# Optimization experiments

Hardware: AMD Instinct MI355X
Metric: run time of the kernel (lower is better)

Reference implementation:

```python
import jax, jax.numpy as jnp
import numpy as np

BATCH, WIDTH, HEIGHT, DEPTH = 1024, 256, 256, 8


def setup_inputs() -> dict:
    key = jax.random.key(0)
    k_val, k_m1, k_b1, k_m2, k_b2 = jax.random.split(key, 5)
    return {
        "val": jax.random.normal(k_val, (BATCH, 1), dtype=jnp.float32),
        "M1": jax.random.normal(k_m1, (DEPTH, WIDTH, HEIGHT), dtype=jnp.float32),
        "B1": jax.random.normal(k_b1, (DEPTH, WIDTH, HEIGHT), dtype=jnp.float32),
        "M2": jax.random.normal(k_m2, (DEPTH, WIDTH, HEIGHT), dtype=jnp.float32),
        "B2": jax.random.normal(k_b2, (DEPTH, WIDTH, HEIGHT), dtype=jnp.float32),
    }


def _run_branch(q0, M, B):
    # q0: [B]; M, B: [depth, W, H]. Sequential recurrence over depth.
    def step(q, mb):
        m, b = mb  # [W, H]
        s = q[:, None, None] * m[None] + b[None]        # [B, W, H]
        q_new = jnp.min(jnp.max(s, axis=-1), axis=-1)    # max over H, then min over W -> [B]
        return q_new, None

    q_final, _ = jax.lax.scan(step, q0, (M, B))
    return q_final


def reference(val, M1, B1, M2, B2):
    q0 = val[:, 0]  # val: [B, 1] -> [B]
    q1 = _run_branch(q0, M1, B1)
    q2 = _run_branch(q0, M2, B2)
    return q1[:, None], q2[:, None]  # each [B, 1], matching torch squeeze(-1) of [B,1,1]
```

## Files before the change

kernel.cpp:

```cpp
#include <hip/hip_runtime.h>
#include <math.h>

#define WH     256
#define NDEPTH 8
#define NBATCH 1024
#define NB     8
#define PLANE  (WH * WH)

typedef _Float16 h2 __attribute__((ext_vector_type(2)));

#define SLAB   (32 * WH)
#define HQ8BLK (NDEPTH * SLAB)

__global__ __launch_bounds__(256) void transpose_half_k(const float* __restrict__ M1,
                                                        const float* __restrict__ B1,
                                                        const float* __restrict__ M2,
                                                        const float* __restrict__ B2,
                                                        _Float16* __restrict__ wsh) {
    __shared__ float tile[64][65];
    const int bid = blockIdx.x;
    const int arr = bid >> 7;
    const int d   = (bid >> 4) & 7;
    const int ht  = (bid >> 2) & 3;
    const int wt  = bid & 3;

    const float* src = (arr == 0) ? M1 : (arr == 1) ? B1 : (arr == 2) ? M2 : B2;
    const float* s = src + d * PLANE;
    _Float16* ob = wsh + (size_t)((arr * 8 + ht * 2) * NDEPTH + d) * SLAB;

    const int t   = threadIdx.x;
    const int q16 = t >> 4;
    const int r16 = t & 15;

#pragma unroll
    for (int p = 0; p < 4; ++p) {
        const int wrow = q16 + p * 16;
        const float4 v = *(const float4*)(s + (wt * 64 + wrow) * WH + ht * 64 + r16 * 4);
        tile[wrow][r16 * 4 + 0] = v.x;
        tile[wrow][r16 * 4 + 1] = v.y;
        tile[wrow][r16 * 4 + 2] = v.z;
        tile[wrow][r16 * 4 + 3] = v.w;
    }
    __syncthreads();
#pragma unroll
    for (int p = 0; p < 4; ++p) {
        const int hrow = q16 + p * 16;
        const int sub  = p >> 1;
        const int hs   = q16 + (p & 1) * 16;
        const int wl   = r16 * 4;
        union { _Float16 f[4]; uint2 u; } pk;
        pk.f[0] = (_Float16)tile[wl + 0][hrow];
        pk.f[1] = (_Float16)tile[wl + 1][hrow];
        pk.f[2] = (_Float16)tile[wl + 2][hrow];
        pk.f[3] = (_Float16)tile[wl + 3][hrow];
        *(uint2*)(ob + (size_t)sub * HQ8BLK + hs * WH + wt * 64 + wl) = pk.u;
    }
}

__global__ __launch_bounds__(512) void prop_h_k(const _Float16* __restrict__ wsh,
                                                const float* __restrict__ val,
                                                float* __restrict__ out) {
    const int bid  = blockIdx.x;
    const int x    = bid & 7;
    const int br   = x >> 2;
    const int bg   = (bid >> 3) * 4 + (x & 3);
    const int t    = threadIdx.x;
    const int wave = t >> 6;
    const int lane = t & 63;

    const int arrM = br ? 2 : 0;
    const int arrB = br ? 3 : 1;
    const uint4* __restrict__ mp = (const uint4*)wsh + (size_t)(arrM * 8 + wave) * (HQ8BLK / 8) + lane;
    const uint4* __restrict__ bp = (const uint4*)wsh + (size_t)(arrB * 8 + wave) * (HQ8BLK / 8) + lane;

    h2 q2[NB];
#pragma unroll
    for (int nb = 0; nb < NB; ++nb) {
        const _Float16 qh = (_Float16)val[bg * NB + nb];
        q2[nb].x = qh; q2[nb].y = qh;
    }

    __shared__ h2 part[8][NB][128];
    __shared__ float qs[NB];

    union H8 { uint4 u; h2 h[4]; };

    uint4 bm[4][2], bb[4][2];
#pragma unroll
    for (int s = 0; s < 3; ++s) {
        bm[s][0] = mp[0]; bm[s][1] = mp[64];
        bb[s][0] = bp[0]; bb[s][1] = bp[64];
        mp += 128; bp += 128;
    }

    union { unsigned short us; _Float16 f; } ninf; ninf.us = 0xFC00;
    h2 NEGINF; NEGINF.x = ninf.f; NEGINF.y = ninf.f;

    for (int d = 0; d < NDEPTH; ++d) {
        h2 acc[NB][4];
#pragma unroll
        for (int nb = 0; nb < NB; ++nb)
#pragma unroll
            for (int k = 0; k < 4; ++k) acc[nb][k] = NEGINF;

#pragma unroll
        for (int c = 0; c < 8; ++c) {
            const int slot = c & 3;
            const int ps   = (c + 3) & 3;
            bm[ps][0] = mp[0]; bm[ps][1] = mp[64];
            bb[ps][0] = bp[0]; bb[ps][1] = bp[64];
            mp += 128; bp += 128;

            H8 m0, m1, b0, b1;
            m0.u = bm[slot][0]; m1.u = bm[slot][1];
            b0.u = bb[slot][0]; b1.u = bb[slot][1];
#pragma unroll
            for (int nb = 0; nb < NB; ++nb) {
                const h2 qq = q2[nb];
#pragma unroll
                for (int k = 0; k < 4; ++k) {
                    acc[nb][k] = __builtin_elementwise_max(
                        acc[nb][k], __builtin_elementwise_fma(qq, m0.h[k], b0.h[k]));
                    acc[nb][k] = __builtin_elementwise_max(
                        acc[nb][k], __builtin_elementwise_fma(qq, m1.h[k], b1.h[k]));
                }
            }
        }

        union IH { int i; h2 h; };
#pragma unroll
        for (int nb = 0; nb < NB; ++nb)
#pragma unroll
            for (int k = 0; k < 4; ++k) {
                IH a; a.h = acc[nb][k];
                IH o2; o2.i = __shfl_xor(a.i, 32);
                acc[nb][k] = __builtin_elementwise_max(acc[nb][k], o2.h);
            }

        if (lane < 32) {
#pragma unroll
            for (int nb = 0; nb < NB; ++nb) {
                H8 st;
                st.h[0] = acc[nb][0]; st.h[1] = acc[nb][1];
                st.h[2] = acc[nb][2]; st.h[3] = acc[nb][3];
                *(uint4*)&part[wave][nb][lane * 4] = st.u;
            }
        }
        __syncthreads();

        if (t < 256) {
            const int nb = t >> 5;
            const int j  = t & 31;
            H8 v; v.u = *(const uint4*)&part[0][nb][j * 4];
#pragma unroll
            for (int s2 = 1; s2 < 8; ++s2) {
                H8 w2; w2.u = *(const uint4*)&part[s2][nb][j * 4];
#pragma unroll
                for (int k = 0; k < 4; ++k)
                    v.h[k] = __builtin_elementwise_max(v.h[k], w2.h[k]);
            }
            h2 mn = __builtin_elementwise_min(
                        __builtin_elementwise_min(v.h[0], v.h[1]),
                        __builtin_elementwise_min(v.h[2], v.h[3]));
            float r = fminf((float)mn.x, (float)mn.y);
#pragma unroll
            for (int off = 16; off > 0; off >>= 1)
                r = fminf(r, __shfl_xor(r, off, 32));
            if (j == 0) qs[nb] = r;
        }
        __syncthreads();
#pragma unroll
        for (int nb = 0; nb < NB; ++nb) {
            const _Float16 qh = (_Float16)qs[nb];
            q2[nb].x = qh; q2[nb].y = qh;
        }
    }

    if (t < NB) out[br * NBATCH + bg * NB + t] = qs[t];
}

extern "C" void kernel_launch(void* const* d_in, const int* in_sizes, int n_in,
                              void* d_out, int out_size, void* d_ws, size_t ws_size,
                              hipStream_t stream) {
    const float* val = (const float*)d_in[0];
    const float* M1  = (const float*)d_in[1];
    const float* B1  = (const float*)d_in[2];
    const float* M2  = (const float*)d_in[3];
    const float* B2  = (const float*)d_in[4];
    float*    out = (float*)d_out;
    _Float16* wsh = (_Float16*)d_ws;

    transpose_half_k<<<dim3(512), dim3(256), 0, stream>>>(M1, B1, M2, B2, wsh);
    prop_h_k<<<dim3(256), dim3(512), 0, stream>>>(wsh, val, out);
}
```

Baseline: 114.8 us.

## Stream weight slabs into LDS via global_load_lds with triple-buffered prefetch

Replaces the 4-deep register prefetch of the M/B half-precision slabs in the propagation kernel with direct global-to-LDS loads (global_load_lds, 16 bytes per lane) into a per-wave 3-slot ring in dynamic shared memory. Explicit vmcnt waits and scheduling barriers control when each slot is consumed. The goal is to free the many VGPRs held by the register ring and keep loads in flight without tying up registers. The two __syncthreads are also replaced with manual lgkmcnt waits plus s_barrier. The cost is extra LDS reads per chunk, a 96 KB dynamic LDS allocation, and fragile hand-written wait counts.

```diff
diff --git a/kernel.cpp b/kernel.cpp
--- a/kernel.cpp
+++ b/kernel.cpp
@@ -57,6 +57,13 @@
     }
 }
 
+
+#define AS1 __attribute__((address_space(1)))
+#define AS3 __attribute__((address_space(3)))
+__device__ __forceinline__ void glds16(const void* g, void* l) {
+    __builtin_amdgcn_global_load_lds((const AS1 void*)g, (AS3 void*)l, 16, 0, 0);
+}
+
 __global__ __launch_bounds__(512) void prop_h_k(const _Float16* __restrict__ wsh,
                                                 const float* __restrict__ val,
                                                 float* __restrict__ out) {
@@ -73,6 +80,13 @@
     const uint4* __restrict__ mp = (const uint4*)wsh + (size_t)(arrM * 8 + wave) * (HQ8BLK / 8) + lane;
     const uint4* __restrict__ bp = (const uint4*)wsh + (size_t)(arrB * 8 + wave) * (HQ8BLK / 8) + lane;
 
+    extern __shared__ uint4 smS[];
+    uint4 (* __restrict__ smM)[3][128] = (uint4(*)[3][128])smS;
+    uint4 (* __restrict__ smB)[3][128] = (uint4(*)[3][128])(smS + 8 * 3 * 128);
+
+    __shared__ h2 part[8][NB][128];
+    __shared__ float qs[NB];
+
     h2 q2[NB];
 #pragma unroll
     for (int nb = 0; nb < NB; ++nb) {
@@ -80,18 +94,18 @@
         q2[nb].x = qh; q2[nb].y = qh;
     }
 
-    __shared__ h2 part[8][NB][128];
-    __shared__ float qs[NB];
-
     union H8 { uint4 u; h2 h[4]; };
 
-    uint4 bm[4][2], bb[4][2];
-#pragma unroll
-    for (int s = 0; s < 3; ++s) {
-        bm[s][0] = mp[0]; bm[s][1] = mp[64];
-        bb[s][0] = bp[0]; bb[s][1] = bp[64];
+#pragma unroll
+    for (int s = 0; s < 2; ++s) {
+        glds16(mp,      &smM[wave][s][0]);
+        glds16(mp + 64, &smM[wave][s][64]);
+        glds16(bp,      &smB[wave][s][0]);
+        glds16(bp + 64, &smB[wave][s][64]);
         mp += 128; bp += 128;
     }
+    int cs = 0;
+    int ps = 2;
 
     union { unsigned short us; _Float16 f; } ninf; ninf.us = 0xFC00;
     h2 NEGINF; NEGINF.x = ninf.f; NEGINF.y = ninf.f;
@@ -105,15 +119,20 @@
 
 #pragma unroll
         for (int c = 0; c < 8; ++c) {
-            const int slot = c & 3;
-            const int ps   = (c + 3) & 3;
-            bm[ps][0] = mp[0]; bm[ps][1] = mp[64];
-            bb[ps][0] = bp[0]; bb[ps][1] = bp[64];
+            glds16(mp,      &smM[wave][ps][0]);
+            glds16(mp + 64, &smM[wave][ps][64]);
+            glds16(bp,      &smB[wave][ps][0]);
+            glds16(bp + 64, &smB[wave][ps][64]);
             mp += 128; bp += 128;
 
+            asm volatile("s_waitcnt vmcnt(8)" ::: "memory");
+            __builtin_amdgcn_sched_barrier(0);
+
+            const uint4* sM = &smM[wave][cs][0];
+            const uint4* sB = &smB[wave][cs][0];
             H8 m0, m1, b0, b1;
-            m0.u = bm[slot][0]; m1.u = bm[slot][1];
-            b0.u = bb[slot][0]; b1.u = bb[slot][1];
+            m0.u = sM[lane]; m1.u = sM[lane + 64];
+            b0.u = sB[lane]; b1.u = sB[lane + 64];
 #pragma unroll
             for (int nb = 0; nb < NB; ++nb) {
                 const h2 qq = q2[nb];
@@ -125,6 +144,8 @@
                         acc[nb][k], __builtin_elementwise_fma(qq, m1.h[k], b1.h[k]));
                 }
             }
+            cs = (cs == 2) ? 0 : cs + 1;
+            ps = (ps == 2) ? 0 : ps + 1;
         }
 
         union IH { int i; h2 h; };
@@ -146,7 +167,8 @@
                 *(uint4*)&part[wave][nb][lane * 4] = st.u;
             }
         }
-        __syncthreads();
+        asm volatile("s_waitcnt lgkmcnt(0)" ::: "memory");
+        __builtin_amdgcn_s_barrier();
 
         if (t < 256) {
             const int nb = t >> 5;
@@ -168,7 +190,8 @@
                 r = fminf(r, __shfl_xor(r, off, 32));
             if (j == 0) qs[nb] = r;
         }
-        __syncthreads();
+        asm volatile("s_waitcnt lgkmcnt(0)" ::: "memory");
+        __builtin_amdgcn_s_barrier();
 #pragma unroll
         for (int nb = 0; nb < NB; ++nb) {
             const _Float16 qh = (_Float16)qs[nb];
@@ -190,6 +213,13 @@
     float*    out = (float*)d_out;
     _Float16* wsh = (_Float16*)d_ws;
 
+    static int smem_set = 0;
+    if (!smem_set) {
+        hipFuncSetAttribute((const void*)prop_h_k,
+                            hipFuncAttributeMaxDynamicSharedMemorySize, 96 * 1024);
+        smem_set = 1;
+    }
+
     transpose_half_k<<<dim3(512), dim3(256), 0, stream>>>(M1, B1, M2, B2, wsh);
-    prop_h_k<<<dim3(256), dim3(512), 0, stream>>>(wsh, val, out);
-}
+    prop_h_k<<<dim3(256), dim3(512), 96 * 1024, stream>>>(wsh, val, out);
+}
```

Result: slower. 124.0 us (+8.0%).

## Split W dimension across paired blocks with atomic exchange, double batch per block

Applied to the files above, without the earlier changes.

Each block now handles 16 batch elements but only half of the W range, so a pair of blocks (bid and bid^8) cover the full plane. The two halves exchange their per-depth partial minima through a global mailbox using atomicExch and spin-wait, and the mailbox is zeroed in the transpose kernel. Doubling the batch per block halves the number of times M/B are streamed per batch element, and the W split keeps the grid size the same. The cost is inter-block spin synchronization, which can deadlock if partner blocks are not co-resident, plus higher register pressure from the 16-wide accumulators.

```diff
diff --git a/kernel.cpp b/kernel.cpp
--- a/kernel.cpp
+++ b/kernel.cpp
@@ -4,21 +4,27 @@
 #define WH     256
 #define NDEPTH 8
 #define NBATCH 1024
-#define NB     8
+#define NB     16
 #define PLANE  (WH * WH)
 
 typedef _Float16 h2 __attribute__((ext_vector_type(2)));
 
 #define SLAB   (32 * WH)
 #define HQ8BLK (NDEPTH * SLAB)
+#define XBUF_OFF (6u * 1024u * 1024u)
 
 __global__ __launch_bounds__(256) void transpose_half_k(const float* __restrict__ M1,
                                                         const float* __restrict__ B1,
                                                         const float* __restrict__ M2,
                                                         const float* __restrict__ B2,
-                                                        _Float16* __restrict__ wsh) {
+                                                        _Float16* __restrict__ wsh,
+                                                        unsigned long long* __restrict__ xbuf) {
     __shared__ float tile[64][65];
     const int bid = blockIdx.x;
+
+    if (bid < 256 && threadIdx.x < NB)
+        xbuf[bid * NB + threadIdx.x] = 0ULL;
+
     const int arr = bid >> 7;
     const int d   = (bid >> 4) & 7;
     const int ht  = (bid >> 2) & 3;
@@ -57,21 +63,29 @@
     }
 }
 
-__global__ __launch_bounds__(512) void prop_h_k(const _Float16* __restrict__ wsh,
-                                                const float* __restrict__ val,
-                                                float* __restrict__ out) {
+__global__ __launch_bounds__(512, 2) void prop_h_k(const _Float16* __restrict__ wsh,
+                                                   const float* __restrict__ val,
+                                                   float* __restrict__ out,
+                                                   unsigned long long* __restrict__ xbuf) {
     const int bid  = blockIdx.x;
     const int x    = bid & 7;
     const int br   = x >> 2;
-    const int bg   = (bid >> 3) * 4 + (x & 3);
+    const int wh   = (bid >> 3) & 1;
+    const int bg   = (bid >> 4) * 4 + (x & 3);
     const int t    = threadIdx.x;
     const int wave = t >> 6;
     const int lane = t & 63;
 
     const int arrM = br ? 2 : 0;
     const int arrB = br ? 3 : 1;
-    const uint4* __restrict__ mp = (const uint4*)wsh + (size_t)(arrM * 8 + wave) * (HQ8BLK / 8) + lane;
-    const uint4* __restrict__ bp = (const uint4*)wsh + (size_t)(arrB * 8 + wave) * (HQ8BLK / 8) + lane;
+    const uint2* __restrict__ mp = (const uint2*)wsh + (size_t)(arrM * 8 + wave) * (HQ8BLK / 4)
+                                   + (lane >> 5) * 64 + wh * 32 + (lane & 31);
+    const uint2* __restrict__ bp = (const uint2*)wsh + (size_t)(arrB * 8 + wave) * (HQ8BLK / 4)
+                                   + (lane >> 5) * 64 + wh * 32 + (lane & 31);
+
+    __shared__ uint2 part[8][NB][32];
+    __shared__ float qsp[NB];
+    __shared__ float qs[NB];
 
     h2 q2[NB];
 #pragma unroll
@@ -80,22 +94,14 @@
         q2[nb].x = qh; q2[nb].y = qh;
     }
 
-    __shared__ h2 part[8][NB][128];
-    __shared__ float qs[NB];
-
-    union H8 { uint4 u; h2 h[4]; };
-
-    uint4 bm[4][2], bb[4][2];
-#pragma unroll
-    for (int s = 0; s < 3; ++s) {
-        bm[s][0] = mp[0]; bm[s][1] = mp[64];
-        bb[s][0] = bp[0]; bb[s][1] = bp[64];
-        mp += 128; bp += 128;
-    }
-
+    union U2 { uint2 u; h2 h[2]; };
+    union IH { int i; h2 h; };
     union { unsigned short us; _Float16 f; } ninf; ninf.us = 0xFC00;
     h2 NEGINF; NEGINF.x = ninf.f; NEGINF.y = ninf.f;
 
+    unsigned long long* xmine = xbuf + bid * NB;
+    unsigned long long* xpart = xbuf + (bid ^ 8) * NB;
+
     for (int d = 0; d < NDEPTH; ++d) {
         h2 acc[NB][4];
 #pragma unroll
@@ -105,68 +111,73 @@
 
 #pragma unroll
         for (int c = 0; c < 8; ++c) {
-            const int slot = c & 3;
-            const int ps   = (c + 3) & 3;
-            bm[ps][0] = mp[0]; bm[ps][1] = mp[64];
-            bb[ps][0] = bp[0]; bb[ps][1] = bp[64];
-            mp += 128; bp += 128;
-
-            H8 m0, m1, b0, b1;
-            m0.u = bm[slot][0]; m1.u = bm[slot][1];
-            b0.u = bb[slot][0]; b1.u = bb[slot][1];
+            U2 m0, m1, b0, b1;
+            m0.u = mp[0]; m1.u = mp[128];
+            b0.u = bp[0]; b1.u = bp[128];
+            mp += 256; bp += 256;
 #pragma unroll
             for (int nb = 0; nb < NB; ++nb) {
                 const h2 qq = q2[nb];
-#pragma unroll
-                for (int k = 0; k < 4; ++k) {
-                    acc[nb][k] = __builtin_elementwise_max(
-                        acc[nb][k], __builtin_elementwise_fma(qq, m0.h[k], b0.h[k]));
-                    acc[nb][k] = __builtin_elementwise_max(
-                        acc[nb][k], __builtin_elementwise_fma(qq, m1.h[k], b1.h[k]));
+                acc[nb][0] = __builtin_elementwise_max(
+                    acc[nb][0], __builtin_elementwise_fma(qq, m0.h[0], b0.h[0]));
+                acc[nb][1] = __builtin_elementwise_max(
+                    acc[nb][1], __builtin_elementwise_fma(qq, m0.h[1], b0.h[1]));
+                acc[nb][2] = __builtin_elementwise_max(
+                    acc[nb][2], __builtin_elementwise_fma(qq, m1.h[0], b1.h[0]));
+                acc[nb][3] = __builtin_elementwise_max(
+                    acc[nb][3], __builtin_elementwise_fma(qq, m1.h[1], b1.h[1]));
+            }
+        }
+
+        if (true) {
+#pragma unroll
+            for (int nb = 0; nb < NB; ++nb) {
+                h2 a0 = __builtin_elementwise_max(acc[nb][0], acc[nb][2]);
+                h2 a1 = __builtin_elementwise_max(acc[nb][1], acc[nb][3]);
+                IH ia, ob0, ob1;
+                ia.h = a0; ob0.i = __shfl_xor(ia.i, 32);
+                ia.h = a1; ob1.i = __shfl_xor(ia.i, 32);
+                a0 = __builtin_elementwise_max(a0, ob0.h);
+                a1 = __builtin_elementwise_max(a1, ob1.h);
+                if (lane < 32) {
+                    U2 st; st.h[0] = a0; st.h[1] = a1;
+                    part[wave][nb][lane] = st.u;
                 }
             }
         }
-
-        union IH { int i; h2 h; };
-#pragma unroll
-        for (int nb = 0; nb < NB; ++nb)
-#pragma unroll
-            for (int k = 0; k < 4; ++k) {
-                IH a; a.h = acc[nb][k];
-                IH o2; o2.i = __shfl_xor(a.i, 32);
-                acc[nb][k] = __builtin_elementwise_max(acc[nb][k], o2.h);
-            }
-
-        if (lane < 32) {
-#pragma unroll
-            for (int nb = 0; nb < NB; ++nb) {
-                H8 st;
-                st.h[0] = acc[nb][0]; st.h[1] = acc[nb][1];
-                st.h[2] = acc[nb][2]; st.h[3] = acc[nb][3];
-                *(uint4*)&part[wave][nb][lane * 4] = st.u;
-            }
-        }
         __syncthreads();
 
-        if (t < 256) {
+        {
             const int nb = t >> 5;
             const int j  = t & 31;
-            H8 v; v.u = *(const uint4*)&part[0][nb][j * 4];
+            U2 v; v.u = part[0][nb][j];
 #pragma unroll
             for (int s2 = 1; s2 < 8; ++s2) {
-                H8 w2; w2.u = *(const uint4*)&part[s2][nb][j * 4];
-#pragma unroll
-                for (int k = 0; k < 4; ++k)
-                    v.h[k] = __builtin_elementwise_max(v.h[k], w2.h[k]);
-            }
-            h2 mn = __builtin_elementwise_min(
-                        __builtin_elementwise_min(v.h[0], v.h[1]),
-                        __builtin_elementwise_min(v.h[2], v.h[3]));
+                U2 w2; w2.u = part[s2][nb][j];
+                v.h[0] = __builtin_elementwise_max(v.h[0], w2.h[0]);
+                v.h[1] = __builtin_elementwise_max(v.h[1], w2.h[1]);
+            }
+            h2 mn = __builtin_elementwise_min(v.h[0], v.h[1]);
             float r = fminf((float)mn.x, (float)mn.y);
 #pragma unroll
             for (int off = 16; off > 0; off >>= 1)
                 r = fminf(r, __shfl_xor(r, off, 32));
-            if (j == 0) qs[nb] = r;
+            if (j == 0) qsp[nb] = r;
+        }
+        __syncthreads();
+
+        if (t < NB) {
+            union { float f; unsigned u; } pv; pv.f = qsp[t];
+            atomicExch(&xmine[t],
+                       ((unsigned long long)pv.u << 32) | (unsigned)(d + 1));
+            unsigned long long got;
+            for (;;) {
+                got = atomicExch(&xpart[t], 0ULL);
+                if ((unsigned)(got & 0xFFFFFFFFULL) == (unsigned)(d + 1)) break;
+                __builtin_amdgcn_s_sleep(1);
+            }
+            union { unsigned u; float f; } qv; qv.u = (unsigned)(got >> 32);
+            qs[t] = fminf(qsp[t], qv.f);
         }
         __syncthreads();
 #pragma unroll
@@ -176,7 +187,7 @@
         }
     }
 
-    if (t < NB) out[br * NBATCH + bg * NB + t] = qs[t];
+    if (wh == 0 && t < NB) out[br * NBATCH + bg * NB + t] = qs[t];
 }
 
 extern "C" void kernel_launch(void* const* d_in, const int* in_sizes, int n_in,
@@ -189,7 +200,9 @@
     const float* B2  = (const float*)d_in[4];
     float*    out = (float*)d_out;
     _Float16* wsh = (_Float16*)d_ws;
-
-    transpose_half_k<<<dim3(512), dim3(256), 0, stream>>>(M1, B1, M2, B2, wsh);
-    prop_h_k<<<dim3(256), dim3(512), 0, stream>>>(wsh, val, out);
+    unsigned long long* xbuf =
+        (unsigned long long*)((char*)d_ws + XBUF_OFF);
+
+    transpose_half_k<<<dim3(512), dim3(256), 0, stream>>>(M1, B1, M2, B2, wsh, xbuf);
+    prop_h_k<<<dim3(256), dim3(512), 0, stream>>>(wsh, val, out, xbuf);
 }
```

After: 130.1 us. 13.3% more time.

## Split W across block pairs with cross-block flag exchange, double batch per block

Applied to the files above, without the earlier changes.

Each block now handles 16 batch elements instead of 8, and the W dimension is split between two paired blocks. The pair exchanges per-depth partial minima through global memory, using release/acquire atomic flags and a spin-wait. This halves each block's weight reads per depth step while reusing every loaded weight across twice as many batch elements. The cost is higher register pressure, the removal of the software prefetch ring, and a deadlock risk if both blocks of a pair are not resident on the GPU at the same time.

```diff
diff --git a/kernel.cpp b/kernel.cpp
--- a/kernel.cpp
+++ b/kernel.cpp
@@ -4,21 +4,27 @@
 #define WH     256
 #define NDEPTH 8
 #define NBATCH 1024
-#define NB     8
+#define NB     16
 #define PLANE  (WH * WH)
 
 typedef _Float16 h2 __attribute__((ext_vector_type(2)));
 
 #define SLAB   (32 * WH)
 #define HQ8BLK (NDEPTH * SLAB)
+#define XBUF_OFF (6u * 1024u * 1024u)
 
 __global__ __launch_bounds__(256) void transpose_half_k(const float* __restrict__ M1,
                                                         const float* __restrict__ B1,
                                                         const float* __restrict__ M2,
                                                         const float* __restrict__ B2,
-                                                        _Float16* __restrict__ wsh) {
+                                                        _Float16* __restrict__ wsh,
+                                                        unsigned long long* __restrict__ xbuf) {
     __shared__ float tile[64][65];
     const int bid = blockIdx.x;
+
+    if (bid < 256 && threadIdx.x < NB)
+        xbuf[bid * NB + threadIdx.x] = 0ULL;
+
     const int arr = bid >> 7;
     const int d   = (bid >> 4) & 7;
     const int ht  = (bid >> 2) & 3;
@@ -57,21 +63,30 @@
     }
 }
 
-__global__ __launch_bounds__(512) void prop_h_k(const _Float16* __restrict__ wsh,
-                                                const float* __restrict__ val,
-                                                float* __restrict__ out) {
+__global__ __launch_bounds__(512, 2) void prop_h_k(const _Float16* __restrict__ wsh,
+                                                   const float* __restrict__ val,
+                                                   float* __restrict__ out,
+                                                   unsigned long long* __restrict__ xbuf) {
     const int bid  = blockIdx.x;
     const int x    = bid & 7;
     const int br   = x >> 2;
-    const int bg   = (bid >> 3) * 4 + (x & 3);
+    const int wh   = (bid >> 3) & 1;
+    const int bg   = (bid >> 4) * 4 + (x & 3);
     const int t    = threadIdx.x;
     const int wave = t >> 6;
     const int lane = t & 63;
+    const int cls  = lane >> 4;
+    const int j16  = lane & 15;
 
     const int arrM = br ? 2 : 0;
     const int arrB = br ? 3 : 1;
-    const uint4* __restrict__ mp = (const uint4*)wsh + (size_t)(arrM * 8 + wave) * (HQ8BLK / 8) + lane;
-    const uint4* __restrict__ bp = (const uint4*)wsh + (size_t)(arrB * 8 + wave) * (HQ8BLK / 8) + lane;
+    const uint4* __restrict__ mp = (const uint4*)wsh + (size_t)(arrM * 8 + wave) * (HQ8BLK / 8)
+                                   + cls * 32 + wh * 16 + j16;
+    const uint4* __restrict__ bp = (const uint4*)wsh + (size_t)(arrB * 8 + wave) * (HQ8BLK / 8)
+                                   + cls * 32 + wh * 16 + j16;
+
+    __shared__ uint4 part[8][NB][16];
+    __shared__ float qs[NB];
 
     h2 q2[NB];
 #pragma unroll
@@ -80,22 +95,14 @@
         q2[nb].x = qh; q2[nb].y = qh;
     }
 
-    __shared__ h2 part[8][NB][128];
-    __shared__ float qs[NB];
-
     union H8 { uint4 u; h2 h[4]; };
-
-    uint4 bm[4][2], bb[4][2];
-#pragma unroll
-    for (int s = 0; s < 3; ++s) {
-        bm[s][0] = mp[0]; bm[s][1] = mp[64];
-        bb[s][0] = bp[0]; bb[s][1] = bp[64];
-        mp += 128; bp += 128;
-    }
-
+    union IH { int i; h2 h; };
     union { unsigned short us; _Float16 f; } ninf; ninf.us = 0xFC00;
     h2 NEGINF; NEGINF.x = ninf.f; NEGINF.y = ninf.f;
 
+    unsigned long long* xmine = xbuf + bid * NB;
+    unsigned long long* xpart = xbuf + (bid ^ 8) * NB;
+
     for (int d = 0; d < NDEPTH; ++d) {
         h2 acc[NB][4];
 #pragma unroll
@@ -104,16 +111,11 @@
             for (int k = 0; k < 4; ++k) acc[nb][k] = NEGINF;
 
 #pragma unroll
-        for (int c = 0; c < 8; ++c) {
-            const int slot = c & 3;
-            const int ps   = (c + 3) & 3;
-            bm[ps][0] = mp[0]; bm[ps][1] = mp[64];
-            bb[ps][0] = bp[0]; bb[ps][1] = bp[64];
-            mp += 128; bp += 128;
-
+        for (int c = 0; c < 4; ++c) {
             H8 m0, m1, b0, b1;
-            m0.u = bm[slot][0]; m1.u = bm[slot][1];
-            b0.u = bb[slot][0]; b1.u = bb[slot][1];
+            m0.u = mp[0]; m1.u = mp[128];
+            b0.u = bp[0]; b1.u = bp[128];
+            mp += 256; bp += 256;
 #pragma unroll
             for (int nb = 0; nb < NB; ++nb) {
                 const h2 qq = q2[nb];
@@ -127,34 +129,36 @@
             }
         }
 
-        union IH { int i; h2 h; };
 #pragma unroll
         for (int nb = 0; nb < NB; ++nb)
 #pragma unroll
             for (int k = 0; k < 4; ++k) {
-                IH a; a.h = acc[nb][k];
-                IH o2; o2.i = __shfl_xor(a.i, 32);
-                acc[nb][k] = __builtin_elementwise_max(acc[nb][k], o2.h);
-            }
-
-        if (lane < 32) {
-#pragma unroll
-            for (int nb = 0; nb < NB; ++nb) {
+                IH a, o1, o2;
+                a.h = acc[nb][k];
+                o1.i = __shfl_xor(a.i, 16);
+                a.h = __builtin_elementwise_max(a.h, o1.h);
+                o2.i = __shfl_xor(a.i, 32);
+                acc[nb][k] = __builtin_elementwise_max(a.h, o2.h);
+            }
+
+#pragma unroll
+        for (int nb = 0; nb < NB; ++nb) {
+            if (cls == (nb >> 2)) {
                 H8 st;
                 st.h[0] = acc[nb][0]; st.h[1] = acc[nb][1];
                 st.h[2] = acc[nb][2]; st.h[3] = acc[nb][3];
-                *(uint4*)&part[wave][nb][lane * 4] = st.u;
+                part[wave][nb][j16] = st.u;
             }
         }
         __syncthreads();
 
         if (t < 256) {
-            const int nb = t >> 5;
-            const int j  = t & 31;
-            H8 v; v.u = *(const uint4*)&part[0][nb][j * 4];
+            const int nb = t >> 4;
+            const int j  = t & 15;
+            H8 v; v.u = part[0][nb][j];
 #pragma unroll
             for (int s2 = 1; s2 < 8; ++s2) {
-                H8 w2; w2.u = *(const uint4*)&part[s2][nb][j * 4];
+                H8 w2; w2.u = part[s2][nb][j];
 #pragma unroll
                 for (int k = 0; k < 4; ++k)
                     v.h[k] = __builtin_elementwise_max(v.h[k], w2.h[k]);
@@ -164,9 +168,24 @@
                         __builtin_elementwise_min(v.h[2], v.h[3]));
             float r = fminf((float)mn.x, (float)mn.y);
 #pragma unroll
-            for (int off = 16; off > 0; off >>= 1)
-                r = fminf(r, __shfl_xor(r, off, 32));
-            if (j == 0) qs[nb] = r;
+            for (int off = 8; off > 0; off >>= 1)
+                r = fminf(r, __shfl_xor(r, off, 16));
+
+            if (j == 0) {
+                union { float f; unsigned u; } pv; pv.f = r;
+                __hip_atomic_store(&xmine[nb],
+                                   ((unsigned long long)pv.u << 32) | (unsigned)(d + 1),
+                                   __ATOMIC_RELEASE, __HIP_MEMORY_SCOPE_AGENT);
+                unsigned long long got;
+                for (;;) {
+                    got = __hip_atomic_load(&xpart[nb], __ATOMIC_ACQUIRE,
+                                            __HIP_MEMORY_SCOPE_AGENT);
+                    if ((unsigned)(got & 0xFFFFFFFFULL) == (unsigned)(d + 1)) break;
+                    __builtin_amdgcn_s_sleep(1);
+                }
+                union { unsigned u; float f; } qv; qv.u = (unsigned)(got >> 32);
+                qs[nb] = fminf(r, qv.f);
+            }
         }
         __syncthreads();
 #pragma unroll
@@ -176,7 +195,7 @@
         }
     }
 
-    if (t < NB) out[br * NBATCH + bg * NB + t] = qs[t];
+    if (wh == 0 && t < NB) out[br * NBATCH + bg * NB + t] = qs[t];
 }
 
 extern "C" void kernel_launch(void* const* d_in, const int* in_sizes, int n_in,
@@ -189,7 +208,9 @@
     const float* B2  = (const float*)d_in[4];
     float*    out = (float*)d_out;
     _Float16* wsh = (_Float16*)d_ws;
-
-    transpose_half_k<<<dim3(512), dim3(256), 0, stream>>>(M1, B1, M2, B2, wsh);
-    prop_h_k<<<dim3(256), dim3(512), 0, stream>>>(wsh, val, out);
+    unsigned long long* xbuf =
+        (unsigned long long*)((char*)d_ws + XBUF_OFF);
+
+    transpose_half_k<<<dim3(512), dim3(256), 0, stream>>>(M1, B1, M2, B2, wsh, xbuf);
+    prop_h_k<<<dim3(256), dim3(512), 0, stream>>>(wsh, val, out, xbuf);
 }
```

New measurement: 276.2 us. 141% more time.
